# Optimization experiments

Hardware: AMD Instinct MI355X
Metric: run time of the kernel (lower is better)

## Reference

```python
import jax, jax.numpy as jnp
import numpy as np

H, R, B, T = 512, 4, 16, 4096

def _glorot(key, shape):
    return jax.random.uniform(key, shape, minval=-1.0, maxval=1.0) * jnp.sqrt(2.0 / sum(shape))

def setup_inputs() -> dict:
    key = jax.random.key(0)
    k1, k2, k3, k4, k5 = jax.random.split(key, 5)
    return {
        "x_seq": jax.random.normal(k5, (B, T, H), dtype=jnp.float32),
        "a_diag": _glorot(k1, (H,)).astype(jnp.float32),
        "p_vec": _glorot(k2, (H, R)).astype(jnp.float32),
        "q_vec": _glorot(k3, (H, R)).astype(jnp.float32),
        "b_mat": _glorot(k4, (H, H)).astype(jnp.float32),
    }

def reference(x_seq, a_diag, p_vec, q_vec, b_mat):
    # A = diag(a_diag) + P Q^T  (DPLR structure, materialized as in the source)
    A = jnp.diag(a_diag) + p_vec @ q_vec.T            # [H, H]
    # Precompute B @ x_t for all timesteps/batches: bx[b,t,k] = sum_h b_mat[k,h] x[b,t,h]
    bx = jnp.einsum("bth,kh->btk", x_seq, b_mat)      # [B, T, H]
    h0 = jnp.zeros((x_seq.shape[0], a_diag.shape[0]), dtype=x_seq.dtype)  # [B, H]

    def step(h, bx_t):
        # h_{t} = A h_{t-1} + B x_t, batched: (h @ A^T)
        h = h @ A.T + bx_t
        return h, h

    _, h_seq = jax.lax.scan(step, h0, jnp.swapaxes(bx, 0, 1))  # [T, B, H]
    return jnp.swapaxes(h_seq, 0, 1)                            # [B, T, H]
```

## Files before the change

### kernel.cpp

```cpp
#include <hip/hip_runtime.h>
#include <hip/hip_bf16.h>

#define H 512
#define RNK 4
#define BATCH 16
#define TT 4096
#define MTOT (BATCH * TT)

#define BM 128
#define BN 128
#define BK 64

#define NCHUNK 128
#define JWARM 32

#define LDK 72

typedef __attribute__((ext_vector_type(8))) short bf16x8;
typedef __attribute__((ext_vector_type(4))) float f32x4;

__device__ inline unsigned short f2bf(float f) {
    unsigned u = __float_as_uint(f);
    u += 0x7FFFu + ((u >> 16) & 1u);
    return (unsigned short)(u >> 16);
}
__device__ inline float bflo(unsigned w) { return __uint_as_float(w << 16); }
__device__ inline float bfhi(unsigned w) { return __uint_as_float(w & 0xFFFF0000u); }

__global__ __launch_bounds__(256) void convert_kernel(
    const float* __restrict__ src, unsigned short* __restrict__ dst, int n4)
{
    int i = blockIdx.x * blockDim.x + threadIdx.x;
    const int stride = gridDim.x * blockDim.x;
    for (; i < n4; i += stride) {
        float4 v = ((const float4*)src)[i];
        ushort4 o = { f2bf(v.x), f2bf(v.y), f2bf(v.z), f2bf(v.w) };
        ((ushort4*)dst)[i] = o;
    }
}

__global__ __launch_bounds__(256) void gemm_bt_kernel(
    const unsigned short* __restrict__ A,
    const unsigned short* __restrict__ Bm,
    unsigned short* __restrict__ C)
{
    __shared__ unsigned short As[BM * BK];
    __shared__ unsigned short Bs[BN * BK];
    const int tid  = threadIdx.x;
    const int lane = tid & 63;
    const int wave = tid >> 6;
    const int wm = (wave >> 1) * 64;
    const int wn = (wave & 1) * 64;
    const size_t m0 = (size_t)blockIdx.x * BM;
    const int n0 = blockIdx.y * BN;
    const int r  = lane & 15;
    const int qd = lane >> 4;

    f32x4 acc[4][4];
    #pragma unroll
    for (int i = 0; i < 4; ++i)
        #pragma unroll
        for (int j = 0; j < 4; ++j)
            acc[i][j] = (f32x4){0.f, 0.f, 0.f, 0.f};

    for (int k0 = 0; k0 < H; k0 += BK) {
        #pragma unroll
        for (int s = 0; s < 4; ++s) {
            const int seg = wave * 4 + s;
            const int off = seg * 1024 + lane * 16;
            const int row = off >> 7;
            const int inrow = off & 127;
            const char* ga = (const char*)(A + (m0 + row) * H + k0) + inrow;
            const char* gb = (const char*)(Bm + (size_t)(n0 + row) * H + k0) + inrow;
            __builtin_amdgcn_global_load_lds(
                (const __attribute__((address_space(1))) unsigned int*)ga,
                (__attribute__((address_space(3))) unsigned int*)&As[seg * 512], 16, 0, 0);
            __builtin_amdgcn_global_load_lds(
                (const __attribute__((address_space(1))) unsigned int*)gb,
                (__attribute__((address_space(3))) unsigned int*)&Bs[seg * 512], 16, 0, 0);
        }
        __syncthreads();
        #pragma unroll
        for (int kk = 0; kk < BK; kk += 32) {
            bf16x8 af[4], bfr[4];
            #pragma unroll
            for (int i = 0; i < 4; ++i)
                af[i] = *(const bf16x8*)&As[(wm + i * 16 + r) * BK + kk + qd * 8];
            #pragma unroll
            for (int j = 0; j < 4; ++j)
                bfr[j] = *(const bf16x8*)&Bs[(wn + j * 16 + r) * BK + kk + qd * 8];
            #pragma unroll
            for (int i = 0; i < 4; ++i)
                #pragma unroll
                for (int j = 0; j < 4; ++j)
                    acc[i][j] = __builtin_amdgcn_mfma_f32_16x16x32_bf16(
                        af[i], bfr[j], acc[i][j], 0, 0, 0);
        }
        __syncthreads();
    }
    #pragma unroll
    for (int i = 0; i < 4; ++i)
        #pragma unroll
        for (int j = 0; j < 4; ++j)
            #pragma unroll
            for (int e = 0; e < 4; ++e) {
                const size_t m = m0 + wm + i * 16 + qd * 4 + e;
                const int n = n0 + wn + j * 16 + r;
                C[m * H + n] = f2bf(acc[i][j][e]);
            }
}

__global__ __launch_bounds__(64) void scan_bf_kernel(
    const unsigned short* __restrict__ bx, float* __restrict__ out,
    const float* __restrict__ a_diag, const float* __restrict__ p_vec,
    const float* __restrict__ q_vec, int nchunk, int warm_max)
{
    const int lane = threadIdx.x;
    const int c = blockIdx.x;
    const int b = blockIdx.y;
    const int L = TT / nchunk;
    const int d0 = lane * 8;

    float ak[8], hk[8];
    float4 pk[8], qk[8];
    #pragma unroll
    for (int j = 0; j < 8; ++j) {
        ak[j] = a_diag[d0 + j];
        pk[j] = *(const float4*)(p_vec + (d0 + j) * RNK);
        qk[j] = *(const float4*)(q_vec + (d0 + j) * RNK);
        hk[j] = 0.f;
    }
    const int warm  = (c == 0) ? 0 : warm_max;
    const int steps = warm + L;
    const int tstart = c * L - warm;
    const unsigned short* src = bx + (size_t)b * TT * H + d0;
    float* dst = out + (size_t)b * TT * H + d0;

    uint4 ring[4];
    #pragma unroll
    for (int i = 0; i < 4; ++i)
        ring[i] = *(const uint4*)(src + (size_t)(tstart + i) * H);

    #pragma unroll 4
    for (int i = 0; i < steps; ++i) {
        const uint4 cur = ring[i & 3];
        if (i + 4 < steps)
            ring[i & 3] = *(const uint4*)(src + (size_t)(tstart + i + 4) * H);
        float u[8];
        u[0] = bflo(cur.x); u[1] = bfhi(cur.x);
        u[2] = bflo(cur.y); u[3] = bfhi(cur.y);
        u[4] = bflo(cur.z); u[5] = bfhi(cur.z);
        u[6] = bflo(cur.w); u[7] = bfhi(cur.w);

        float s0 = 0.f, s1 = 0.f, s2 = 0.f, s3 = 0.f;
        #pragma unroll
        for (int j = 0; j < 8; ++j) {
            s0 += qk[j].x * hk[j]; s1 += qk[j].y * hk[j];
            s2 += qk[j].z * hk[j]; s3 += qk[j].w * hk[j];
        }
        #pragma unroll
        for (int off = 32; off > 0; off >>= 1) {
            s0 += __shfl_xor(s0, off); s1 += __shfl_xor(s1, off);
            s2 += __shfl_xor(s2, off); s3 += __shfl_xor(s3, off);
        }
        #pragma unroll
        for (int j = 0; j < 8; ++j)
            hk[j] = ak[j] * hk[j] + (pk[j].x * s0 + pk[j].y * s1 + pk[j].z * s2 + pk[j].w * s3) + u[j];
        if (i >= warm) {
            float* d = dst + (size_t)(tstart + i) * H;
            *(float4*)d = (float4){hk[0], hk[1], hk[2], hk[3]};
            *(float4*)(d + 4) = (float4){hk[4], hk[5], hk[6], hk[7]};
        }
    }
}

__global__ __launch_bounds__(256) void gemm_fused_kernel(
    const float* __restrict__ X, const float* __restrict__ W, float* __restrict__ bx)
{
    __shared__ unsigned short As[BM * LDK];
    __shared__ unsigned short Bs[BN * LDK];
    const int tid  = threadIdx.x;
    const int lane = tid & 63;
    const int wave = tid >> 6;
    const int wm = (wave >> 1) * 64;
    const int wn = (wave & 1) * 64;
    const size_t mbase = (size_t)blockIdx.x * BM;
    const int nbase = blockIdx.y * BN;
    const float* Xb = X + mbase * H;
    const float* Wb = W + (size_t)nbase * H;
    f32x4 acc[4][4];
    #pragma unroll
    for (int i = 0; i < 4; ++i)
        #pragma unroll
        for (int j = 0; j < 4; ++j)
            acc[i][j] = (f32x4){0.f, 0.f, 0.f, 0.f};
    const int r  = lane & 15;
    const int qd = lane >> 4;
    for (int k0 = 0; k0 < H; k0 += BK) {
        #pragma unroll
        for (int i = 0; i < 8; ++i) {
            int idx = tid + i * 256;
            int row = idx >> 4;
            int c4  = (idx & 15) * 4;
            float4 va = *(const float4*)(Xb + (size_t)row * H + k0 + c4);
            float4 vb = *(const float4*)(Wb + (size_t)row * H + k0 + c4);
            ushort4 wa = { f2bf(va.x), f2bf(va.y), f2bf(va.z), f2bf(va.w) };
            ushort4 wb = { f2bf(vb.x), f2bf(vb.y), f2bf(vb.z), f2bf(vb.w) };
            *(ushort4*)&As[row * LDK + c4] = wa;
            *(ushort4*)&Bs[row * LDK + c4] = wb;
        }
        __syncthreads();
        #pragma unroll
        for (int kk = 0; kk < BK; kk += 32) {
            bf16x8 af[4], bfr[4];
            #pragma unroll
            for (int i = 0; i < 4; ++i)
                af[i] = *(const bf16x8*)&As[(wm + i * 16 + r) * LDK + kk + qd * 8];
            #pragma unroll
            for (int j = 0; j < 4; ++j)
                bfr[j] = *(const bf16x8*)&Bs[(wn + j * 16 + r) * LDK + kk + qd * 8];
            #pragma unroll
            for (int i = 0; i < 4; ++i)
                #pragma unroll
                for (int j = 0; j < 4; ++j)
                    acc[i][j] = __builtin_amdgcn_mfma_f32_16x16x32_bf16(
                        af[i], bfr[j], acc[i][j], 0, 0, 0);
        }
        __syncthreads();
    }
    #pragma unroll
    for (int i = 0; i < 4; ++i)
        #pragma unroll
        for (int j = 0; j < 4; ++j)
            #pragma unroll
            for (int e = 0; e < 4; ++e) {
                int m = wm + i * 16 + qd * 4 + e;
                int n = wn + j * 16 + r;
                bx[(mbase + m) * H + nbase + n] = acc[i][j][e];
            }
}

__global__ __launch_bounds__(64) void scan_f32_kernel(
    const float* __restrict__ bx, float* __restrict__ out,
    const float* __restrict__ a_diag, const float* __restrict__ p_vec,
    const float* __restrict__ q_vec)
{
    const int lane = threadIdx.x;
    const int b = blockIdx.y;
    const int d0 = lane * 8;
    float ak[8], hk[8];
    float4 pk[8], qk[8];
    #pragma unroll
    for (int j = 0; j < 8; ++j) {
        ak[j] = a_diag[d0 + j];
        pk[j] = *(const float4*)(p_vec + (d0 + j) * RNK);
        qk[j] = *(const float4*)(q_vec + (d0 + j) * RNK);
        hk[j] = 0.f;
    }
    const float* src = bx + (size_t)b * TT * H + d0;
    float* dst = out + (size_t)b * TT * H + d0;
    for (int i = 0; i < TT; ++i) {
        const float* sp = src + (size_t)i * H;
        float4 va = *(const float4*)sp, vb = *(const float4*)(sp + 4);
        float u[8] = {va.x, va.y, va.z, va.w, vb.x, vb.y, vb.z, vb.w};
        float s0 = 0.f, s1 = 0.f, s2 = 0.f, s3 = 0.f;
        #pragma unroll
        for (int j = 0; j < 8; ++j) {
            s0 += qk[j].x * hk[j]; s1 += qk[j].y * hk[j];
            s2 += qk[j].z * hk[j]; s3 += qk[j].w * hk[j];
        }
        #pragma unroll
        for (int off = 32; off > 0; off >>= 1) {
            s0 += __shfl_xor(s0, off); s1 += __shfl_xor(s1, off);
            s2 += __shfl_xor(s2, off); s3 += __shfl_xor(s3, off);
        }
        #pragma unroll
        for (int j = 0; j < 8; ++j)
            hk[j] = ak[j] * hk[j] + (pk[j].x * s0 + pk[j].y * s1 + pk[j].z * s2 + pk[j].w * s3) + u[j];
        float* d = dst + (size_t)i * H;
        *(float4*)d = (float4){hk[0], hk[1], hk[2], hk[3]};
        *(float4*)(d + 4) = (float4){hk[4], hk[5], hk[6], hk[7]};
    }
}

extern "C" void kernel_launch(void* const* d_in, const int* in_sizes, int n_in,
                              void* d_out, int out_size, void* d_ws, size_t ws_size,
                              hipStream_t stream) {
    (void)in_sizes; (void)n_in; (void)out_size;
    const float* x = (const float*)d_in[0];
    const float* a = (const float*)d_in[1];
    const float* p = (const float*)d_in[2];
    const float* q = (const float*)d_in[3];
    const float* w = (const float*)d_in[4];
    float* out = (float*)d_out;

    const size_t nx    = (size_t)MTOT * H;
    const size_t xbf_b = nx * 2;
    const size_t wbf_b = (size_t)H * H * 2;
    const size_t bxb_b = nx * 2;

    unsigned short *xbf = nullptr, *wbf = nullptr, *bxbf = nullptr;
    if (ws_size >= xbf_b + wbf_b + bxb_b) {
        xbf  = (unsigned short*)d_ws;
        wbf  = xbf + nx;
        bxbf = wbf + (size_t)H * H;
    } else if (ws_size >= bxb_b) {
        xbf  = (unsigned short*)d_out;
        wbf  = xbf + nx;
        bxbf = (unsigned short*)d_ws;
    }

    if (bxbf != nullptr) {
        convert_kernel<<<8192, 256, 0, stream>>>(x, xbf, (int)(nx / 4));
        convert_kernel<<<256, 256, 0, stream>>>(w, wbf, (int)(H * H / 4));
        dim3 g1(MTOT / BM, H / BN), b1(256);
        gemm_bt_kernel<<<g1, b1, 0, stream>>>(xbf, wbf, bxbf);
        dim3 g2(NCHUNK, BATCH), b2(64);
        scan_bf_kernel<<<g2, b2, 0, stream>>>(bxbf, out, a, p, q, NCHUNK, JWARM);
    } else {
        dim3 g1(MTOT / BM, H / BN), b1(256);
        gemm_fused_kernel<<<g1, b1, 0, stream>>>(x, w, out);
        dim3 g2(1, BATCH), b2(64);
        scan_f32_kernel<<<g2, b2, 0, stream>>>(out, out, a, p, q);
    }
}
```

Baseline: 372.2 us.

## Block four scan steps to batch cross-lane reductions via DPLR algebra

Restructures the sequential scan to process four timesteps per block. It splits the state into a diagonal-only recurrence plus a low-rank correction, using precomputed Q^T diag(a)^k P matrices, so the four butterfly reductions run together and the wave-wide shuffle latency is paid once per four steps instead of every step. This adds more arithmetic per step and more registers. It also changes the floating-point summation order and assumes the step count is a multiple of four.

New measurement: 342.5 us. 8.0% less time.

```diff
diff --git a/kernel.cpp b/kernel.cpp
--- a/kernel.cpp
+++ b/kernel.cpp
@@ -26,6 +26,9 @@
 }
 __device__ inline float bflo(unsigned w) { return __uint_as_float(w << 16); }
 __device__ inline float bfhi(unsigned w) { return __uint_as_float(w & 0xFFFF0000u); }
+__device__ inline float rfl(float x) {
+    return __uint_as_float(__builtin_amdgcn_readfirstlane(__float_as_uint(x)));
+}
 
 __global__ __launch_bounds__(256) void convert_kernel(
     const float* __restrict__ src, unsigned short* __restrict__ dst, int n4)
@@ -121,56 +124,156 @@
     const int L = TT / nchunk;
     const int d0 = lane * 8;
 
-    float ak[8], hk[8];
+    float ak[8], g[8];
     float4 pk[8], qk[8];
     #pragma unroll
     for (int j = 0; j < 8; ++j) {
         ak[j] = a_diag[d0 + j];
         pk[j] = *(const float4*)(p_vec + (d0 + j) * RNK);
         qk[j] = *(const float4*)(q_vec + (d0 + j) * RNK);
-        hk[j] = 0.f;
-    }
+        g[j] = 0.f;
+    }
+
+    float Gx[3][4][4];
+    {
+        float part[3][16];
+        #pragma unroll
+        for (int k = 0; k < 3; ++k)
+            #pragma unroll
+            for (int v = 0; v < 16; ++v) part[k][v] = 0.f;
+        #pragma unroll
+        for (int d = 0; d < 8; ++d) {
+            const float a1 = ak[d], a2 = a1 * a1;
+            const float qr[4] = {qk[d].x, qk[d].y, qk[d].z, qk[d].w};
+            const float pc[4] = {pk[d].x, pk[d].y, pk[d].z, pk[d].w};
+            #pragma unroll
+            for (int r = 0; r < 4; ++r)
+                #pragma unroll
+                for (int cc = 0; cc < 4; ++cc) {
+                    const float qp = qr[r] * pc[cc];
+                    part[0][r * 4 + cc] += qp;
+                    part[1][r * 4 + cc] += qp * a1;
+                    part[2][r * 4 + cc] += qp * a2;
+                }
+        }
+        #pragma unroll
+        for (int off = 32; off > 0; off >>= 1)
+            #pragma unroll
+            for (int k = 0; k < 3; ++k)
+                #pragma unroll
+                for (int v = 0; v < 16; ++v)
+                    part[k][v] += __shfl_xor(part[k][v], off);
+        #pragma unroll
+        for (int k = 0; k < 3; ++k)
+            #pragma unroll
+            for (int r = 0; r < 4; ++r)
+                #pragma unroll
+                for (int cc = 0; cc < 4; ++cc)
+                    Gx[k][r][cc] = rfl(part[k][r * 4 + cc]);
+    }
+
     const int warm  = (c == 0) ? 0 : warm_max;
     const int steps = warm + L;
+    const int nb    = steps >> 2;
     const int tstart = c * L - warm;
     const unsigned short* src = bx + (size_t)b * TT * H + d0;
     float* dst = out + (size_t)b * TT * H + d0;
 
     uint4 ring[4];
     #pragma unroll
-    for (int i = 0; i < 4; ++i)
-        ring[i] = *(const uint4*)(src + (size_t)(tstart + i) * H);
-
-    #pragma unroll 4
-    for (int i = 0; i < steps; ++i) {
-        const uint4 cur = ring[i & 3];
-        if (i + 4 < steps)
-            ring[i & 3] = *(const uint4*)(src + (size_t)(tstart + i + 4) * H);
-        float u[8];
-        u[0] = bflo(cur.x); u[1] = bfhi(cur.x);
-        u[2] = bflo(cur.y); u[3] = bfhi(cur.y);
-        u[4] = bflo(cur.z); u[5] = bfhi(cur.z);
-        u[6] = bflo(cur.w); u[7] = bfhi(cur.w);
-
-        float s0 = 0.f, s1 = 0.f, s2 = 0.f, s3 = 0.f;
-        #pragma unroll
-        for (int j = 0; j < 8; ++j) {
-            s0 += qk[j].x * hk[j]; s1 += qk[j].y * hk[j];
-            s2 += qk[j].z * hk[j]; s3 += qk[j].w * hk[j];
-        }
-        #pragma unroll
-        for (int off = 32; off > 0; off >>= 1) {
-            s0 += __shfl_xor(s0, off); s1 += __shfl_xor(s1, off);
-            s2 += __shfl_xor(s2, off); s3 += __shfl_xor(s3, off);
-        }
-        #pragma unroll
-        for (int j = 0; j < 8; ++j)
-            hk[j] = ak[j] * hk[j] + (pk[j].x * s0 + pk[j].y * s1 + pk[j].z * s2 + pk[j].w * s3) + u[j];
-        if (i >= warm) {
-            float* d = dst + (size_t)(tstart + i) * H;
-            *(float4*)d = (float4){hk[0], hk[1], hk[2], hk[3]};
-            *(float4*)(d + 4) = (float4){hk[4], hk[5], hk[6], hk[7]};
-        }
+    for (int j = 0; j < 4; ++j)
+        ring[j] = *(const uint4*)(src + (size_t)(tstart + j) * H);
+
+    for (int blk = 0; blk < nb; ++blk) {
+        const int i0 = blk * 4;
+        float yp[4][4];
+        float gs[4][8];
+
+        #pragma unroll
+        for (int j = 0; j < 4; ++j) {
+            float y0 = 0.f, y1 = 0.f, y2 = 0.f, y3 = 0.f;
+            #pragma unroll
+            for (int d = 0; d < 8; ++d) {
+                y0 += qk[d].x * g[d]; y1 += qk[d].y * g[d];
+                y2 += qk[d].z * g[d]; y3 += qk[d].w * g[d];
+            }
+            yp[j][0] = y0; yp[j][1] = y1; yp[j][2] = y2; yp[j][3] = y3;
+
+            const uint4 cur = ring[j];
+            int iload = i0 + 4 + j;
+            if (iload > steps - 1) iload = steps - 1;
+            ring[j] = *(const uint4*)(src + (size_t)(tstart + iload) * H);
+
+            float u[8];
+            u[0] = bflo(cur.x); u[1] = bfhi(cur.x);
+            u[2] = bflo(cur.y); u[3] = bfhi(cur.y);
+            u[4] = bflo(cur.z); u[5] = bfhi(cur.z);
+            u[6] = bflo(cur.w); u[7] = bfhi(cur.w);
+            #pragma unroll
+            for (int d = 0; d < 8; ++d) { g[d] = ak[d] * g[d] + u[d]; gs[j][d] = g[d]; }
+        }
+
+        #pragma unroll
+        for (int off = 32; off > 0; off >>= 1)
+            #pragma unroll
+            for (int j = 0; j < 4; ++j)
+                #pragma unroll
+                for (int r = 0; r < 4; ++r)
+                    yp[j][r] += __shfl_xor(yp[j][r], off);
+
+        float sv[4][4];
+        #pragma unroll
+        for (int r = 0; r < 4; ++r) sv[0][r] = yp[0][r];
+        #pragma unroll
+        for (int r = 0; r < 4; ++r) {
+            float t = yp[1][r];
+            #pragma unroll
+            for (int cc = 0; cc < 4; ++cc) t += Gx[0][r][cc] * sv[0][cc];
+            sv[1][r] = t;
+        }
+        #pragma unroll
+        for (int r = 0; r < 4; ++r) {
+            float t = yp[2][r];
+            #pragma unroll
+            for (int cc = 0; cc < 4; ++cc) t += Gx[1][r][cc] * sv[0][cc];
+            #pragma unroll
+            for (int cc = 0; cc < 4; ++cc) t += Gx[0][r][cc] * sv[1][cc];
+            sv[2][r] = t;
+        }
+        #pragma unroll
+        for (int r = 0; r < 4; ++r) {
+            float t = yp[3][r];
+            #pragma unroll
+            for (int cc = 0; cc < 4; ++cc) t += Gx[2][r][cc] * sv[0][cc];
+            #pragma unroll
+            for (int cc = 0; cc < 4; ++cc) t += Gx[1][r][cc] * sv[1][cc];
+            #pragma unroll
+            for (int cc = 0; cc < 4; ++cc) t += Gx[0][r][cc] * sv[2][cc];
+            sv[3][r] = t;
+        }
+
+        const bool dostore = (i0 >= warm);
+        float e[8];
+        #pragma unroll
+        for (int d = 0; d < 8; ++d) e[d] = 0.f;
+        #pragma unroll
+        for (int j = 0; j < 4; ++j) {
+            #pragma unroll
+            for (int d = 0; d < 8; ++d) {
+                const float ps = pk[d].x * sv[j][0] + pk[d].y * sv[j][1]
+                               + pk[d].z * sv[j][2] + pk[d].w * sv[j][3];
+                e[d] = ak[d] * e[d] + ps;
+            }
+            if (dostore) {
+                float* dd = dst + (size_t)(tstart + i0 + j) * H;
+                *(float4*)dd       = (float4){gs[j][0] + e[0], gs[j][1] + e[1],
+                                              gs[j][2] + e[2], gs[j][3] + e[3]};
+                *(float4*)(dd + 4) = (float4){gs[j][4] + e[4], gs[j][5] + e[5],
+                                              gs[j][6] + e[6], gs[j][7] + e[7]};
+            }
+        }
+        #pragma unroll
+        for (int d = 0; d < 8; ++d) g[d] = gs[3][d] + e[d];
     }
 }
 
```
